# Performance work log

Hardware: AMD Instinct MI355X
Metric: run time of the kernel (lower is better)

Reference implementation:

```python
import jax, jax.numpy as jnp
import numpy as np

R_MIN, R_MAX, MAX_PHASE = 0.9, 0.999, 6.283
BN_EPS = 1e-5


def _lru(x, nu_log, theta_log, B_re, B_im, C_re, C_im, D):
    # x: [B,T,E]; diagonal LRU with complex state of size H
    lam = jnp.exp(-jnp.exp(nu_log) + 1j * jnp.exp(theta_log))          # [H] complex
    gamma = jnp.sqrt(jnp.maximum(1.0 - jnp.abs(lam) ** 2, 1e-12))      # [H]
    Bc = B_re + 1j * B_im                                               # [H,E]
    Cc = C_re + 1j * C_im                                               # [E,H]
    Bu = jnp.einsum('bte,he->bth', x.astype(jnp.complex64), Bc) * gamma  # [B,T,H]

    def step(h, u):
        h = lam * h + u
        return h, h

    h0 = jnp.zeros((x.shape[0], lam.shape[0]), jnp.complex64)
    _, hs = jax.lax.scan(step, h0, jnp.swapaxes(Bu, 0, 1))              # [T,B,H]
    hs = jnp.swapaxes(hs, 0, 1)                                         # [B,T,H]
    return jnp.einsum('bth,eh->bte', hs, Cc).real + D * x               # [B,T,E]


def _batchnorm(x, scale, bias):
    # normalize over (batch, time), feature axis last
    mu = jnp.mean(x, axis=(0, 1))
    var = jnp.var(x, axis=(0, 1))
    return (x - mu) * jax.lax.rsqrt(var + BN_EPS) * scale + bias


def _glu(x):
    a, b = jnp.split(x, 2, axis=-1)
    return a * jax.nn.sigmoid(b)


def setup_inputs() -> dict:
    key = jax.random.key(0)
    ks = jax.random.split(key, 16)
    B, T, TS, E, H, L, O, NB = 32, 2048, 64, 256, 256, 1024, 10, 6
    u1 = jax.random.uniform(ks[0], (NB, H))
    u2 = jax.random.uniform(ks[1], (NB, H))
    nu_log = jnp.log(-0.5 * jnp.log(u1 * (R_MAX**2 - R_MIN**2) + R_MIN**2))
    theta_log = jnp.log(MAX_PHASE * u2)
    return {
        'x': jax.random.normal(ks[2], (B, T, TS), jnp.float32),
        'W_enc': jax.random.normal(ks[3], (TS, E), jnp.float32) / np.sqrt(TS),
        'b_enc': jnp.zeros((E,), jnp.float32),
        'nu_log': nu_log.astype(jnp.float32),
        'theta_log': theta_log.astype(jnp.float32),
        'B_re': jax.random.normal(ks[4], (NB, H, E), jnp.float32) / np.sqrt(2 * E),
        'B_im': jax.random.normal(ks[5], (NB, H, E), jnp.float32) / np.sqrt(2 * E),
        'C_re': jax.random.normal(ks[6], (NB, E, H), jnp.float32) / np.sqrt(H),
        'C_im': jax.random.normal(ks[7], (NB, E, H), jnp.float32) / np.sqrt(H),
        'D': jax.random.normal(ks[8], (NB, E), jnp.float32),
        'W1': jax.random.normal(ks[9], (NB, E, L), jnp.float32) / np.sqrt(E),
        'b1': jnp.zeros((NB, L), jnp.float32),
        'W2': jax.random.normal(ks[10], (NB, L // 2, E), jnp.float32) / np.sqrt(L // 2),
        'b2': jnp.zeros((NB, E), jnp.float32),
        'bn_scale': jnp.ones((NB, E), jnp.float32),
        'bn_bias': jnp.zeros((NB, E), jnp.float32),
        'W_out': jax.random.normal(ks[11], (E, O), jnp.float32) / np.sqrt(E),
        'b_out': jnp.zeros((O,), jnp.float32),
    }


def reference(x, W_enc, b_enc, nu_log, theta_log, B_re, B_im, C_re, C_im, D,
              W1, b1, W2, b2, bn_scale, bn_bias, W_out, b_out):
    x = x @ W_enc + b_enc                      # [B,T,E]
    y = x                                       # residual anchor (same for every block)
    for i in range(6):
        h = _batchnorm(x, bn_scale[i], bn_bias[i])
        h = _lru(h, nu_log[i], theta_log[i], B_re[i], B_im[i], C_re[i], C_im[i], D[i])
        h = _glu(h @ W1[i] + b1[i])             # dropout is identity (p=0 / eval)
        h = h @ W2[i] + b2[i]
        x = h + y
    pooled = jnp.mean(x, axis=1)                # pool=True head: mean over time
    return pooled @ W_out + b_out               # [B, out_dim]
```

## Files before the change

### kernel.cpp

```cpp
#include <hip/hip_runtime.h>
#include <hip/hip_bf16.h>
#include <math.h>

using bf16 = __hip_bfloat16;
typedef __attribute__((ext_vector_type(8))) short s8v;
typedef __attribute__((ext_vector_type(4))) float f4v;

#define MTOT 65536
#define TLEN 2048
#define NCHUNK 32
#define TCH 64

__device__ __forceinline__ float b2f(bf16 x) { return __bfloat162float(x); }
__device__ __forceinline__ bf16 f2b(float x) { return __float2bfloat16(x); }
__device__ __forceinline__ float bits2f(unsigned short u) {
    unsigned int x = ((unsigned int)u) << 16; float f; __builtin_memcpy(&f, &x, 4); return f;
}
__device__ __forceinline__ unsigned short f2bits(float x) {
    bf16 h = f2b(x); unsigned short u; __builtin_memcpy(&u, &h, 2); return u;
}

__device__ __forceinline__ float ldf(const void* p, size_t i, int f) {
    return f ? ((const float*)p)[i] : b2f(((const bf16*)p)[i]);
}

__device__ __forceinline__ void ld_g2l(const void* g, void* l) {
    __builtin_amdgcn_global_load_lds(
        (const __attribute__((address_space(1))) void*)g,
        (__attribute__((address_space(3))) void*)l,
        16, 0, 0);
}

__global__ void detect_k(const unsigned short* __restrict__ x, int* __restrict__ flag) {
    int tid = threadIdx.x;
    int cnt = 0;
    for (int i = tid; i < 8192; i += 256) {
        int e = (x[i] >> 7) & 0xFF;
        if (e == 0 || e == 0xFF) cnt++;
    }
    __shared__ int red[256];
    red[tid] = cnt;
    __syncthreads();
    for (int s = 128; s > 0; s >>= 1) {
        if (tid < s) red[tid] += red[tid + s];
        __syncthreads();
    }
    if (tid == 0) flag[0] = (red[0] >= 2) ? 1 : 0;
}

__global__ void cvt_k(const void* __restrict__ src, bf16* __restrict__ dst, int n,
                      const int* __restrict__ flag) {
    int f = *flag;
    int i = blockIdx.x * 256 + threadIdx.x;
    if (i < n) dst[i] = f2b(ldf(src, i, f));
}

__global__ void cvt_small(const void* b_enc, const void* Dp, const void* b1, const void* b2,
                          const void* bn_s, const void* bn_b, const void* W_out, const void* b_out,
                          bf16* b_encb, bf16* Db, bf16* b1b, bf16* b2b, bf16* bnsb, bf16* bnbb,
                          bf16* Woutb, bf16* boutb, const int* __restrict__ flag) {
    int f = *flag;
    int blk = blockIdx.x, t = threadIdx.x;
    const void* src; bf16* dst; int base, n;
    if (blk < 1)       { src = b_enc; dst = b_encb; base = blk;      n = 256; }
    else if (blk < 7)  { src = Dp;    dst = Db;     base = blk - 1;  n = 1536; }
    else if (blk < 31) { src = b1;    dst = b1b;    base = blk - 7;  n = 6144; }
    else if (blk < 37) { src = b2;    dst = b2b;    base = blk - 31; n = 1536; }
    else if (blk < 43) { src = bn_s;  dst = bnsb;   base = blk - 37; n = 1536; }
    else if (blk < 49) { src = bn_b;  dst = bnbb;   base = blk - 43; n = 1536; }
    else if (blk < 59) { src = W_out; dst = Woutb;  base = blk - 49; n = 2560; }
    else               { src = b_out; dst = boutb;  base = 0;        n = 10; }
    int i = base * 256 + t;
    if (i < n) dst[i] = f2b(ldf(src, i, f));
}

__global__ void lamgam_k(const void* __restrict__ nu, const void* __restrict__ th,
                         float* __restrict__ lamb, float* __restrict__ gamt,
                         const int* __restrict__ flag) {
    int f = *flag;
    int g = blockIdx.x * 256 + threadIdx.x;
    float nl = ldf(nu, g, f), tl = ldf(th, g, f);
    float mag = expf(-expf(nl));
    float ang = expf(tl);
    lamb[g * 2] = mag * cosf(ang);
    lamb[g * 2 + 1] = mag * sinf(ang);
    gamt[g] = sqrtf(fmaxf(1.f - mag * mag, 1e-12f));
}

template<int KK, int NBN, int EPI>
__global__ __launch_bounds__(256)
void gemm_v7(const bf16* __restrict__ A, const bf16* __restrict__ W,
             bf16* __restrict__ outB, bf16* __restrict__ outB2, int ldo,
             const bf16* __restrict__ bias,
             const bf16* __restrict__ Dv, const bf16* __restrict__ aux,
             const float* __restrict__ fstats, float* __restrict__ spart)
{
    constexpr int LG = (NBN == 8) ? 3 : 2;
    const int id = blockIdx.x;
    const int xcd = id & 7, q = id >> 3;
    const int bn = q & (NBN - 1);
    const int bm = (q >> LG) * 8 + xcd;

    const int tid = threadIdx.x;
    const int lane = tid & 63, wv = tid >> 6;
    const int wm = wv >> 1, wn = wv & 1;
    const int quad = lane >> 4, cl = lane & 15;

    __shared__ __align__(16) short As[3][128 * 32];
    __shared__ __align__(16) short Ws[3][64 * 32];
    __shared__ float sred[256];

    const char* Ab = (const char*)A + (size_t)bm * 128 * ((size_t)KK * 2);
    const char* Wb = (const char*)W + (size_t)bn * 64 * ((size_t)KK * 2);
    constexpr int ldb = KK * 2;

    auto stage = [&](int t, int bi) {
        const int kb = t * 64;
#pragma unroll
        for (int it = 0; it < 2; ++it) {
            int G = it * 256 + tid;
            int r = G >> 2;
            int gl = (G & 3) ^ ((r >> 1) & 3);
            ld_g2l(Ab + (size_t)r * ldb + kb + gl * 16,
                   (char*)As[bi] + (it * 4 + wv) * 1024);
        }
        {
            int r = tid >> 2;
            int gl = (tid & 3) ^ ((r >> 1) & 3);
            ld_g2l(Wb + (size_t)r * ldb + kb + gl * 16,
                   (char*)Ws[bi] + wv * 1024);
        }
    };

    f4v acc[4][2];
#pragma unroll
    for (int i = 0; i < 4; i++)
#pragma unroll
        for (int j = 0; j < 2; j++) acc[i][j] = (f4v){0.f, 0.f, 0.f, 0.f};

    constexpr int NT = KK >> 5;
    stage(0, 0);
    if (NT > 1) stage(1, 1);
#pragma unroll
    for (int t = 0; t < NT; ++t) {
        if (t + 2 < NT) {
            stage(t + 2, (t + 2) % 3);
            asm volatile("s_waitcnt vmcnt(6)" ::: "memory");
        } else if (t + 1 < NT) {
            asm volatile("s_waitcnt vmcnt(3)" ::: "memory");
        } else {
            asm volatile("s_waitcnt vmcnt(0)" ::: "memory");
        }
        asm volatile("s_barrier" ::: "memory");
        const char* Ac = (const char*)As[t % 3];
        const char* Wc = (const char*)Ws[t % 3];
        s8v af[4], bw[2];
#pragma unroll
        for (int i = 0; i < 4; i++) {
            int r = wm * 64 + i * 16 + cl;
            af[i] = *(const s8v*)(Ac + r * 64 + ((quad ^ ((r >> 1) & 3)) * 16));
        }
#pragma unroll
        for (int j = 0; j < 2; j++) {
            int r = wn * 32 + j * 16 + cl;
            bw[j] = *(const s8v*)(Wc + r * 64 + ((quad ^ ((r >> 1) & 3)) * 16));
        }
#pragma unroll
        for (int i = 0; i < 4; i++)
#pragma unroll
            for (int j = 0; j < 2; j++)
                acc[i][j] = __builtin_amdgcn_mfma_f32_16x16x32_bf16(af[i], bw[j], acc[i][j], 0, 0, 0);
        asm volatile("s_barrier" ::: "memory");
    }

    const size_t ld = (size_t)ldo;
    constexpr bool STATS = (EPI == 1 || EPI == 5);
#pragma unroll
    for (int j = 0; j < 2; j++) {
        float ss = 0.f, ss2 = 0.f;
        const int n = bn * 64 + wn * 32 + j * 16 + cl;
#pragma unroll
        for (int i = 0; i < 4; i++) {
#pragma unroll
            for (int r4 = 0; r4 < 4; r4++) {
                int m = bm * 128 + wm * 64 + i * 16 + quad * 4 + r4;
                size_t idx = (size_t)m * ld + n;
                float v = acc[i][j][r4];
                if (EPI == 1) {
                    v += b2f(bias[n]);
                    outB[idx] = f2b(v);
                    outB2[idx] = f2b(v);
                } else if (EPI == 2) {
                    v += b2f(Dv[n]) * (fstats[n] * b2f(aux[idx]) + fstats[256 + n]);
                    outB[idx] = f2b(v);
                } else if (EPI == 5) {
                    v += b2f(bias[n]) + b2f(aux[idx]);
                    outB[idx] = f2b(v);
                } else if (EPI == 6) {
                    v += fstats[n];
                    outB[idx] = f2b(v);
                }
                if (STATS) { ss += v; ss2 += v * v; }
            }
        }
        if (STATS) {
            ss += __shfl_xor(ss, 16);  ss += __shfl_xor(ss, 32);
            ss2 += __shfl_xor(ss2, 16); ss2 += __shfl_xor(ss2, 32);
            if (lane < 16) {
                int nl = wn * 32 + j * 16 + lane;
                sred[wm * 64 + nl] = ss;
                sred[128 + wm * 64 + nl] = ss2;
            }
        }
    }
    if constexpr (STATS) {
        __syncthreads();
        if (tid < 64) {
            float sv = sred[tid] + sred[64 + tid];
            float sv2 = sred[128 + tid] + sred[192 + tid];
            spart[(size_t)bm * 256 + bn * 64 + tid] = sv;
            spart[131072 + (size_t)bm * 256 + bn * 64 + tid] = sv2;
        }
    }
}

__global__ __launch_bounds__(256)
void glu_v7(const bf16* __restrict__ A, const bf16* __restrict__ W,
            bf16* __restrict__ outB, const bf16* __restrict__ bias)
{
    constexpr int KK = 256;
    const int id = blockIdx.x;
    const int xcd = id & 7, q = id >> 3;
    const int nb = q & 7;
    const int bm = (q >> 3) * 8 + xcd;

    const int tid = threadIdx.x;
    const int lane = tid & 63, wv = tid >> 6;
    const int wm = wv >> 1, wn = wv & 1;
    const int quad = lane >> 4, cl = lane & 15;

    __shared__ __align__(16) short As[3][128 * 32];
    __shared__ __align__(16) short Vs[3][64 * 32];
    __shared__ __align__(16) short Gs[3][64 * 32];

    const char* Ab = (const char*)A + (size_t)bm * 128 * ((size_t)KK * 2);
    const char* Vb = (const char*)W + (size_t)(nb * 64) * ((size_t)KK * 2);
    const char* Gb = (const char*)W + (size_t)(512 + nb * 64) * ((size_t)KK * 2);
    constexpr int ldb = KK * 2;

    auto stage = [&](int t, int bi) {
        const int kb = t * 64;
#pragma unroll
        for (int it = 0; it < 2; ++it) {
            int G = it * 256 + tid;
            int r = G >> 2;
            int gl = (G & 3) ^ ((r >> 1) & 3);
            ld_g2l(Ab + (size_t)r * ldb + kb + gl * 16,
                   (char*)As[bi] + (it * 4 + wv) * 1024);
        }
        {
            int r = tid >> 2;
            int gl = (tid & 3) ^ ((r >> 1) & 3);
            ld_g2l(Vb + (size_t)r * ldb + kb + gl * 16, (char*)Vs[bi] + wv * 1024);
            ld_g2l(Gb + (size_t)r * ldb + kb + gl * 16, (char*)Gs[bi] + wv * 1024);
        }
    };

    f4v accv[4][2], accg[4][2];
#pragma unroll
    for (int i = 0; i < 4; i++)
#pragma unroll
        for (int j = 0; j < 2; j++) {
            accv[i][j] = (f4v){0.f, 0.f, 0.f, 0.f};
            accg[i][j] = (f4v){0.f, 0.f, 0.f, 0.f};
        }

    constexpr int NT = KK >> 5;
    stage(0, 0);
    stage(1, 1);
#pragma unroll
    for (int t = 0; t < NT; ++t) {
        if (t + 2 < NT) {
            stage(t + 2, (t + 2) % 3);
            asm volatile("s_waitcnt vmcnt(8)" ::: "memory");
        } else if (t + 1 < NT) {
            asm volatile("s_waitcnt vmcnt(4)" ::: "memory");
        } else {
            asm volatile("s_waitcnt vmcnt(0)" ::: "memory");
        }
        asm volatile("s_barrier" ::: "memory");
        const char* Ac = (const char*)As[t % 3];
        const char* Vc = (const char*)Vs[t % 3];
        const char* Gc = (const char*)Gs[t % 3];
        s8v af[4], bv[2], bg[2];
#pragma unroll
        for (int i = 0; i < 4; i++) {
            int r = wm * 64 + i * 16 + cl;
            af[i] = *(const s8v*)(Ac + r * 64 + ((quad ^ ((r >> 1) & 3)) * 16));
        }
#pragma unroll
        for (int j = 0; j < 2; j++) {
            int r = wn * 32 + j * 16 + cl;
            int off = r * 64 + ((quad ^ ((r >> 1) & 3)) * 16);
            bv[j] = *(const s8v*)(Vc + off);
            bg[j] = *(const s8v*)(Gc + off);
        }
#pragma unroll
        for (int i = 0; i < 4; i++)
#pragma unroll
            for (int j = 0; j < 2; j++) {
                accv[i][j] = __builtin_amdgcn_mfma_f32_16x16x32_bf16(af[i], bv[j], accv[i][j], 0, 0, 0);
                accg[i][j] = __builtin_amdgcn_mfma_f32_16x16x32_bf16(af[i], bg[j], accg[i][j], 0, 0, 0);
            }
        asm volatile("s_barrier" ::: "memory");
    }

#pragma unroll
    for (int i = 0; i < 4; i++) {
#pragma unroll
        for (int j = 0; j < 2; j++) {
#pragma unroll
            for (int r4 = 0; r4 < 4; r4++) {
                int m = bm * 128 + wm * 64 + i * 16 + quad * 4 + r4;
                int n = nb * 64 + wn * 32 + j * 16 + cl;
                float v = accv[i][j][r4] + b2f(bias[n]);
                float g = accg[i][j][r4] + b2f(bias[512 + n]);
                outB[(size_t)m * 512 + n] = f2b(v * (1.f / (1.f + __expf(-g))));
            }
        }
    }
}

__global__ void bn_finish2(const float* __restrict__ part, float* __restrict__ stats,
                           const bf16* __restrict__ sc, const bf16* __restrict__ bi) {
    int e = blockIdx.x;
    int t = threadIdx.x;
    float s = part[(size_t)t * 256 + e] + part[(size_t)(t + 256) * 256 + e];
    float s2 = part[131072 + (size_t)t * 256 + e] + part[131072 + (size_t)(t + 256) * 256 + e];
    __shared__ float rs[256], rs2[256];
    rs[t] = s; rs2[t] = s2;
    __syncthreads();
    for (int k = 128; k > 0; k >>= 1) {
        if (t < k) { rs[t] += rs[t + k]; rs2[t] += rs2[t + k]; }
        __syncthreads();
    }
    if (t == 0) {
        float mu = rs[0] * (1.f / 65536.f);
        float var = rs2[0] * (1.f / 65536.f) - mu * mu;
        float a = rsqrtf(var + 1e-5f) * b2f(sc[e]);
        stats[e] = a;
        stats[256 + e] = b2f(bi[e]) - mu * a;
    }
}

__global__ void pack_wb(const void* __restrict__ B_re, const void* __restrict__ B_im,
                        size_t off, const float* __restrict__ gam,
                        const float* __restrict__ stats,
                        bf16* __restrict__ out, float* __restrict__ bias_out,
                        const int* __restrict__ flag) {
    int f = *flag;
    int n = blockIdx.x;
    int e = threadIdx.x;
    int h = n >> 1;
    const void* src = (n & 1) ? B_im : B_re;
    float v = ldf(src, off + (size_t)h * 256 + e, f);
    out[(size_t)n * 256 + e] = f2b(v * gam[h] * stats[e]);
    __shared__ float rs[256];
    rs[e] = v * stats[256 + e];
    __syncthreads();
    for (int k = 128; k > 0; k >>= 1) {
        if (e < k) rs[e] += rs[e + k];
        __syncthreads();
    }
    if (e == 0) bias_out[n] = rs[0] * gam[h];
}

__global__ void pack_all(const void* __restrict__ C_re, const void* __restrict__ C_im,
                         const void* __restrict__ W1, const void* __restrict__ W2,
                         bf16* __restrict__ wc6, bf16* __restrict__ w1t6, bf16* __restrict__ w2t6,
                         const int* __restrict__ flag) {
    int f = *flag;
    int L = blockIdx.x >> 11;
    int blk = blockIdx.x & 2047;
    size_t offC = (size_t)L * 65536, offW1 = (size_t)L * 262144, offW2 = (size_t)L * 131072;
    if (blk < 512) {
        int g = blk * 256 + threadIdx.x;
        int e = g >> 9, k = g & 511, h = k >> 1;
        float v = ldf((k & 1) ? C_im : C_re, offC + (size_t)e * 256 + h, f);
        wc6[(size_t)L * 131072 + g] = f2b((k & 1) ? -v : v);
    } else if (blk < 1536) {
        int g = (blk - 512) * 256 + threadIdx.x;
        int n = g >> 8, k = g & 255;
        w1t6[(size_t)L * 262144 + g] = f2b(ldf(W1, offW1 + (size_t)k * 1024 + n, f));
    } else {
        int g = (blk - 1536) * 256 + threadIdx.x;
        int n = g >> 9, k = g & 511;
        w2t6[(size_t)L * 131072 + g] = f2b(ldf(W2, offW2 + (size_t)k * 256 + n, f));
    }
}

__global__ void lru_carry(const bf16* __restrict__ bu, const float* __restrict__ lam,
                          float* __restrict__ carry) {
    int gg = blockIdx.x * 256 + threadIdx.x;
    int hp = gg & 127, c = (gg >> 7) & 31, b = gg >> 12;
    f4v lm = *(const f4v*)&lam[hp * 4];
    float sr0 = 0.f, si0 = 0.f, sr1 = 0.f, si1 = 0.f;
    const char* p = (const char*)(bu + ((size_t)(b * TLEN + c * TCH)) * 512) + hp * 8;
    for (int t = 0; t < TCH; t++) {
        unsigned long long u = *(const unsigned long long*)p;
        float ur0 = bits2f((unsigned short)u), ui0 = bits2f((unsigned short)(u >> 16));
        float ur1 = bits2f((unsigned short)(u >> 32)), ui1 = bits2f((unsigned short)(u >> 48));
        float nr0 = lm[0] * sr0 - lm[1] * si0 + ur0;
        si0 = lm[0] * si0 + lm[1] * sr0 + ui0; sr0 = nr0;
        float nr1 = lm[2] * sr1 - lm[3] * si1 + ur1;
        si1 = lm[2] * si1 + lm[3] * sr1 + ui1; sr1 = nr1;
        p += 1024;
    }
    *(f4v*)&carry[(size_t)gg * 4] = (f4v){sr0, si0, sr1, si1};
}

__global__ void lru_prefix(const float* __restrict__ carry, float* __restrict__ pre,
                           const float* __restrict__ lam) {
    int g = blockIdx.x * 256 + threadIdx.x;
    int h = g & 255, b = g >> 8;
    float pr = lam[h * 2], pi = lam[h * 2 + 1];
    for (int k = 0; k < 6; k++) { float nr = pr * pr - pi * pi; pi = 2.f * pr * pi; pr = nr; }
    float er = 0.f, ei = 0.f;
    for (int c = 0; c < NCHUNK; c++) {
        size_t idx = ((size_t)(b * NCHUNK + c) * 256 + h) * 2;
        pre[idx] = er; pre[idx + 1] = ei;
        float cr = carry[idx], ci = carry[idx + 1];
        float nr = pr * er - pi * ei + cr;
        ei = pr * ei + pi * er + ci;
        er = nr;
    }
}

__global__ void lru_final(bf16* __restrict__ bu, const float* __restrict__ pre,
                          const float* __restrict__ lam) {
    int gg = blockIdx.x * 256 + threadIdx.x;
    int hp = gg & 127, c = (gg >> 7) & 31, b = gg >> 12;
    f4v lm = *(const f4v*)&lam[hp * 4];
    f4v st = *(const f4v*)&pre[(size_t)gg * 4];
    float sr0 = st[0], si0 = st[1], sr1 = st[2], si1 = st[3];
    char* p = (char*)(bu + ((size_t)(b * TLEN + c * TCH)) * 512) + hp * 8;
    for (int t = 0; t < TCH; t++) {
        unsigned long long u = *(const unsigned long long*)p;
        float ur0 = bits2f((unsigned short)u), ui0 = bits2f((unsigned short)(u >> 16));
        float ur1 = bits2f((unsigned short)(u >> 32)), ui1 = bits2f((unsigned short)(u >> 48));
        float nr0 = lm[0] * sr0 - lm[1] * si0 + ur0;
        si0 = lm[0] * si0 + lm[1] * sr0 + ui0; sr0 = nr0;
        float nr1 = lm[2] * sr1 - lm[3] * si1 + ur1;
        si1 = lm[2] * si1 + lm[3] * sr1 + ui1; sr1 = nr1;
        unsigned long long w = (unsigned long long)f2bits(sr0)
                             | ((unsigned long long)f2bits(si0) << 16)
                             | ((unsigned long long)f2bits(sr1) << 32)
                             | ((unsigned long long)f2bits(si1) << 48);
        *(unsigned long long*)p = w;
        p += 1024;
    }
}

__global__ void head_k(const float* __restrict__ part, const bf16* __restrict__ W_out,
                       const bf16* __restrict__ b_out, void* __restrict__ out,
                       const int* __restrict__ flag) {
    int b = blockIdx.x;
    int tid = threadIdx.x;
    __shared__ float sp[256];
    __shared__ float red[160];
    float s = 0.f;
    for (int c = 0; c < 16; c++) s += part[((size_t)(b * 16 + c)) * 256 + tid];
    sp[tid] = s * (1.f / 2048.f);
    __syncthreads();
    if (tid < 160) {
        int o = tid >> 4, sg = tid & 15;
        float a = 0.f;
        for (int e = sg; e < 256; e += 16) a += sp[e] * b2f(W_out[e * 10 + o]);
        red[tid] = a;
    }
    __syncthreads();
    if (tid < 10) {
        float acc = b2f(b_out[tid]);
        for (int sg = 0; sg < 16; sg++) acc += red[tid * 16 + sg];
        if (*flag) ((float*)out)[b * 10 + tid] = acc;
        else       ((bf16*)out)[b * 10 + tid] = f2b(acc);
    }
}

__global__ void pack_wt_enc(const void* __restrict__ W_enc, bf16* __restrict__ out,
                            const int* __restrict__ flag) {
    int f = *flag;
    int g = blockIdx.x * 256 + threadIdx.x;
    int n = g >> 6, k = g & 63;
    out[g] = f2b(ldf(W_enc, (size_t)k * 256 + n, f));
}

extern "C" void kernel_launch(void* const* d_in, const int* in_sizes, int n_in,
                              void* d_out, int out_size, void* d_ws, size_t ws_size,
                              hipStream_t stream) {
    (void)in_sizes; (void)n_in; (void)out_size; (void)ws_size;
    const void* x      = d_in[0];
    const void* W_enc  = d_in[1];
    const void* b_enc  = d_in[2];
    const void* nu_log = d_in[3];
    const void* th_log = d_in[4];
    const void* B_re   = d_in[5];
    const void* B_im   = d_in[6];
    const void* C_re   = d_in[7];
    const void* C_im   = d_in[8];
    const void* Dp     = d_in[9];
    const void* W1     = d_in[10];
    const void* b1     = d_in[11];
    const void* W2     = d_in[12];
    const void* b2     = d_in[13];
    const void* bn_s   = d_in[14];
    const void* bn_b   = d_in[15];
    const void* W_out  = d_in[16];
    const void* b_out  = d_in[17];

    char* w = (char*)d_ws;
    bf16* xc  = (bf16*)w; w += (size_t)MTOT * 256 * 2;
    bf16* y   = (bf16*)w; w += (size_t)MTOT * 256 * 2;
    bf16* hbn = (bf16*)w; w += (size_t)MTOT * 256 * 2;
    bf16* bu  = (bf16*)w; w += (size_t)MTOT * 512 * 2;
    float* stats  = (float*)w; w += 4096;
    float* bnpart = (float*)w; w += 1048576;
    float* carry  = (float*)w; w += 2097152;
    float* pre    = (float*)w; w += 2097152;
    float* lamb   = (float*)w; w += 12288;
    float* gamt   = (float*)w; w += 6144;
    float* bubias = (float*)w; w += 2048;
    int*   flag   = (int*)w;  w += 256;
    bf16* wt_enc = (bf16*)w; w += 32768;
    bf16* wb   = (bf16*)w; w += 262144;
    bf16* wc6  = (bf16*)w; w += 6 * 262144;
    bf16* w1t6 = (bf16*)w; w += 6 * 524288;
    bf16* w2t6 = (bf16*)w; w += 6 * 262144;
    bf16* b_encb = (bf16*)w; w += 512;
    bf16* Db     = (bf16*)w; w += 3072;
    bf16* b1b    = (bf16*)w; w += 12288;
    bf16* b2b    = (bf16*)w; w += 3072;
    bf16* bnsb   = (bf16*)w; w += 3072;
    bf16* bnbb   = (bf16*)w; w += 3072;
    bf16* Woutb  = (bf16*)w; w += 5120;
    bf16* boutb  = (bf16*)w; w += 32;
    bf16* xb = bu;

    dim3 blk(256);
    detect_k<<<1, blk, 0, stream>>>((const unsigned short*)x, flag);
    cvt_k<<<16384, blk, 0, stream>>>(x, xb, 4194304, flag);
    cvt_small<<<60, blk, 0, stream>>>(b_enc, Dp, b1, b2, bn_s, bn_b, W_out, b_out,
                                      b_encb, Db, b1b, b2b, bnsb, bnbb, Woutb, boutb, flag);
    lamgam_k<<<6, blk, 0, stream>>>(nu_log, th_log, lamb, gamt, flag);
    pack_wt_enc<<<64, blk, 0, stream>>>(W_enc, wt_enc, flag);
    pack_all<<<12288, blk, 0, stream>>>(C_re, C_im, W1, W2, wc6, w1t6, w2t6, flag);

    gemm_v7<64, 4, 1><<<2048, blk, 0, stream>>>(xb, wt_enc, xc, y, 256,
                                                b_encb, nullptr, nullptr, nullptr, bnpart);
    for (int i = 0; i < 6; ++i) {
        bn_finish2<<<256, blk, 0, stream>>>(bnpart, stats, bnsb + i * 256, bnbb + i * 256);
        pack_wb<<<512, blk, 0, stream>>>(B_re, B_im, (size_t)i * 65536, gamt + i * 256,
                                         stats, wb, bubias, flag);
        gemm_v7<256, 8, 6><<<4096, blk, 0, stream>>>(xc, wb, bu, nullptr, 512,
                                                     nullptr, nullptr, nullptr, bubias, nullptr);
        lru_carry<<<512, blk, 0, stream>>>(bu, lamb + i * 512, carry);
        lru_prefix<<<32, blk, 0, stream>>>(carry, pre, lamb + i * 512);
        lru_final<<<512, blk, 0, stream>>>(bu, pre, lamb + i * 512);
        gemm_v7<512, 4, 2><<<2048, blk, 0, stream>>>(bu, wc6 + (size_t)i * 131072, hbn, nullptr, 256,
                                                     nullptr, Db + i * 256, xc, stats, nullptr);
        glu_v7<<<4096, blk, 0, stream>>>(hbn, w1t6 + (size_t)i * 262144, bu, b1b + i * 1024);
        gemm_v7<512, 4, 5><<<2048, blk, 0, stream>>>(bu, w2t6 + (size_t)i * 131072, xc, nullptr, 256,
                                                     b2b + i * 256, nullptr, y, nullptr, bnpart);
    }
    head_k<<<32, blk, 0, stream>>>(bnpart, Woutb, boutb, d_out, flag);
}
```

Before: 1.393 ms.

## Process two M-tiles per GEMM block with continuous cross-tile prefetch pipeline

Each GEMM and GLU block now handles two consecutive 128-row M tiles. The three-stage LDS pipeline runs across both tiles, so the second tile's loads are prefetched while the first tile finishes and its epilogue is written. Grids are halved to match. The input conversion kernel also handles four elements per thread. The aim is to amortize pipeline fill/drain and launch overhead, at the cost of fewer blocks and a mid-loop epilogue that may lengthen the critical path.

```diff
diff --git a/kernel.cpp b/kernel.cpp
--- a/kernel.cpp
+++ b/kernel.cpp
@@ -48,11 +48,16 @@
     if (tid == 0) flag[0] = (red[0] >= 2) ? 1 : 0;
 }
 
-__global__ void cvt_k(const void* __restrict__ src, bf16* __restrict__ dst, int n,
-                      const int* __restrict__ flag) {
+__global__ void cvt_k4(const void* __restrict__ src, bf16* __restrict__ dst, int n,
+                       const int* __restrict__ flag) {
     int f = *flag;
-    int i = blockIdx.x * 256 + threadIdx.x;
-    if (i < n) dst[i] = f2b(ldf(src, i, f));
+    int i = (blockIdx.x * 256 + threadIdx.x) * 4;
+    if (i + 3 < n) {
+#pragma unroll
+        for (int k = 0; k < 4; k++) dst[i + k] = f2b(ldf(src, i + k, f));
+    } else {
+        for (int k = 0; k < 4 && i + k < n; k++) dst[i + k] = f2b(ldf(src, i + k, f));
+    }
 }
 
 __global__ void cvt_small(const void* b_enc, const void* Dp, const void* b1, const void* b2,
@@ -89,17 +94,21 @@
 
 template<int KK, int NBN, int EPI>
 __global__ __launch_bounds__(256)
-void gemm_v7(const bf16* __restrict__ A, const bf16* __restrict__ W,
+void gemm_v8(const bf16* __restrict__ A, const bf16* __restrict__ W,
              bf16* __restrict__ outB, bf16* __restrict__ outB2, int ldo,
              const bf16* __restrict__ bias,
              const bf16* __restrict__ Dv, const bf16* __restrict__ aux,
              const float* __restrict__ fstats, float* __restrict__ spart)
 {
     constexpr int LG = (NBN == 8) ? 3 : 2;
+    constexpr int NT = KK >> 5;
+    constexpr int LOG2NT = (KK == 64) ? 1 : (KK == 256) ? 3 : 4;
+    constexpr int GT = 2 * NT;
+
     const int id = blockIdx.x;
     const int xcd = id & 7, q = id >> 3;
     const int bn = q & (NBN - 1);
-    const int bm = (q >> LG) * 8 + xcd;
+    const int mgrp = (q >> LG) * 8 + xcd;
 
     const int tid = threadIdx.x;
     const int lane = tid & 63, wv = tid >> 6;
@@ -110,17 +119,20 @@
     __shared__ __align__(16) short Ws[3][64 * 32];
     __shared__ float sred[256];
 
-    const char* Ab = (const char*)A + (size_t)bm * 128 * ((size_t)KK * 2);
+    const char* Abase = (const char*)A;
     const char* Wb = (const char*)W + (size_t)bn * 64 * ((size_t)KK * 2);
     constexpr int ldb = KK * 2;
 
-    auto stage = [&](int t, int bi) {
-        const int kb = t * 64;
+    auto stage = [&](int G) {
+        const int tile = G >> LOG2NT;
+        const int kb = (G & (NT - 1)) * 64;
+        const int bi = G % 3;
+        const char* Ab = Abase + (size_t)(mgrp * 2 + tile) * 128 * ((size_t)KK * 2);
 #pragma unroll
         for (int it = 0; it < 2; ++it) {
-            int G = it * 256 + tid;
-            int r = G >> 2;
-            int gl = (G & 3) ^ ((r >> 1) & 3);
+            int Gt = it * 256 + tid;
+            int r = Gt >> 2;
+            int gl = (Gt & 3) ^ ((r >> 1) & 3);
             ld_g2l(Ab + (size_t)r * ldb + kb + gl * 16,
                    (char*)As[bi] + (it * 4 + wv) * 1024);
         }
@@ -138,22 +150,24 @@
 #pragma unroll
         for (int j = 0; j < 2; j++) acc[i][j] = (f4v){0.f, 0.f, 0.f, 0.f};
 
-    constexpr int NT = KK >> 5;
-    stage(0, 0);
-    if (NT > 1) stage(1, 1);
-#pragma unroll
-    for (int t = 0; t < NT; ++t) {
-        if (t + 2 < NT) {
-            stage(t + 2, (t + 2) % 3);
+    const size_t ld = (size_t)ldo;
+    constexpr bool STATS = (EPI == 1 || EPI == 5);
+
+    stage(0);
+    stage(1);
+#pragma unroll
+    for (int G = 0; G < GT; ++G) {
+        if (G + 2 < GT) {
+            stage(G + 2);
             asm volatile("s_waitcnt vmcnt(6)" ::: "memory");
-        } else if (t + 1 < NT) {
+        } else if (G + 1 < GT) {
             asm volatile("s_waitcnt vmcnt(3)" ::: "memory");
         } else {
             asm volatile("s_waitcnt vmcnt(0)" ::: "memory");
         }
         asm volatile("s_barrier" ::: "memory");
-        const char* Ac = (const char*)As[t % 3];
-        const char* Wc = (const char*)Ws[t % 3];
+        const char* Ac = (const char*)As[G % 3];
+        const char* Wc = (const char*)Ws[G % 3];
         s8v af[4], bw[2];
 #pragma unroll
         for (int i = 0; i < 4; i++) {
@@ -171,68 +185,76 @@
             for (int j = 0; j < 2; j++)
                 acc[i][j] = __builtin_amdgcn_mfma_f32_16x16x32_bf16(af[i], bw[j], acc[i][j], 0, 0, 0);
         asm volatile("s_barrier" ::: "memory");
-    }
-
-    const size_t ld = (size_t)ldo;
-    constexpr bool STATS = (EPI == 1 || EPI == 5);
-#pragma unroll
-    for (int j = 0; j < 2; j++) {
-        float ss = 0.f, ss2 = 0.f;
-        const int n = bn * 64 + wn * 32 + j * 16 + cl;
-#pragma unroll
-        for (int i = 0; i < 4; i++) {
-#pragma unroll
-            for (int r4 = 0; r4 < 4; r4++) {
-                int m = bm * 128 + wm * 64 + i * 16 + quad * 4 + r4;
-                size_t idx = (size_t)m * ld + n;
-                float v = acc[i][j][r4];
-                if (EPI == 1) {
-                    v += b2f(bias[n]);
-                    outB[idx] = f2b(v);
-                    outB2[idx] = f2b(v);
-                } else if (EPI == 2) {
-                    v += b2f(Dv[n]) * (fstats[n] * b2f(aux[idx]) + fstats[256 + n]);
-                    outB[idx] = f2b(v);
-                } else if (EPI == 5) {
-                    v += b2f(bias[n]) + b2f(aux[idx]);
-                    outB[idx] = f2b(v);
-                } else if (EPI == 6) {
-                    v += fstats[n];
-                    outB[idx] = f2b(v);
+
+        if ((G & (NT - 1)) == NT - 1) {
+            const int bm = mgrp * 2 + (G >> LOG2NT);
+#pragma unroll
+            for (int j = 0; j < 2; j++) {
+                float ss = 0.f, ss2 = 0.f;
+                const int n = bn * 64 + wn * 32 + j * 16 + cl;
+#pragma unroll
+                for (int i = 0; i < 4; i++) {
+#pragma unroll
+                    for (int r4 = 0; r4 < 4; r4++) {
+                        int m = bm * 128 + wm * 64 + i * 16 + quad * 4 + r4;
+                        size_t idx = (size_t)m * ld + n;
+                        float v = acc[i][j][r4];
+                        if (EPI == 1) {
+                            v += b2f(bias[n]);
+                            outB[idx] = f2b(v);
+                            outB2[idx] = f2b(v);
+                        } else if (EPI == 2) {
+                            v += b2f(Dv[n]) * (fstats[n] * b2f(aux[idx]) + fstats[256 + n]);
+                            outB[idx] = f2b(v);
+                        } else if (EPI == 5) {
+                            v += b2f(bias[n]) + b2f(aux[idx]);
+                            outB[idx] = f2b(v);
+                        } else if (EPI == 6) {
+                            v += fstats[n];
+                            outB[idx] = f2b(v);
+                        }
+                        if (STATS) { ss += v; ss2 += v * v; }
+                    }
                 }
-                if (STATS) { ss += v; ss2 += v * v; }
+                if (STATS) {
+                    ss += __shfl_xor(ss, 16);  ss += __shfl_xor(ss, 32);
+                    ss2 += __shfl_xor(ss2, 16); ss2 += __shfl_xor(ss2, 32);
+                    if (lane < 16) {
+                        int nl = wn * 32 + j * 16 + lane;
+                        sred[wm * 64 + nl] = ss;
+                        sred[128 + wm * 64 + nl] = ss2;
+                    }
+                }
             }
-        }
-        if (STATS) {
-            ss += __shfl_xor(ss, 16);  ss += __shfl_xor(ss, 32);
-            ss2 += __shfl_xor(ss2, 16); ss2 += __shfl_xor(ss2, 32);
-            if (lane < 16) {
-                int nl = wn * 32 + j * 16 + lane;
-                sred[wm * 64 + nl] = ss;
-                sred[128 + wm * 64 + nl] = ss2;
+            if constexpr (STATS) {
+                __syncthreads();
+                if (tid < 64) {
+                    float sv = sred[tid] + sred[64 + tid];
+                    float sv2 = sred[128 + tid] + sred[192 + tid];
+                    spart[(size_t)bm * 256 + bn * 64 + tid] = sv;
+                    spart[131072 + (size_t)bm * 256 + bn * 64 + tid] = sv2;
+                }
             }
-        }
-    }
-    if constexpr (STATS) {
-        __syncthreads();
-        if (tid < 64) {
-            float sv = sred[tid] + sred[64 + tid];
-            float sv2 = sred[128 + tid] + sred[192 + tid];
-            spart[(size_t)bm * 256 + bn * 64 + tid] = sv;
-            spart[131072 + (size_t)bm * 256 + bn * 64 + tid] = sv2;
+            if (G + 1 < GT) {
+#pragma unroll
+                for (int i = 0; i < 4; i++)
+#pragma unroll
+                    for (int j = 0; j < 2; j++) acc[i][j] = (f4v){0.f, 0.f, 0.f, 0.f};
+            }
         }
     }
 }
 
 __global__ __launch_bounds__(256)
-void glu_v7(const bf16* __restrict__ A, const bf16* __restrict__ W,
+void glu_v8(const bf16* __restrict__ A, const bf16* __restrict__ W,
             bf16* __restrict__ outB, const bf16* __restrict__ bias)
 {
     constexpr int KK = 256;
+    constexpr int NT = 8, GT = 16;
     const int id = blockIdx.x;
     const int xcd = id & 7, q = id >> 3;
     const int nb = q & 7;
-    const int bm = (q >> 3) * 8 + xcd;
+    const int mgrp = (q >> 3) * 8 + xcd;
 
     const int tid = threadIdx.x;
     const int lane = tid & 63, wv = tid >> 6;
@@ -243,18 +265,21 @@
     __shared__ __align__(16) short Vs[3][64 * 32];
     __shared__ __align__(16) short Gs[3][64 * 32];
 
-    const char* Ab = (const char*)A + (size_t)bm * 128 * ((size_t)KK * 2);
+    const char* Abase = (const char*)A;
     const char* Vb = (const char*)W + (size_t)(nb * 64) * ((size_t)KK * 2);
     const char* Gb = (const char*)W + (size_t)(512 + nb * 64) * ((size_t)KK * 2);
     constexpr int ldb = KK * 2;
 
-    auto stage = [&](int t, int bi) {
-        const int kb = t * 64;
+    auto stage = [&](int G) {
+        const int tile = G >> 3;
+        const int kb = (G & 7) * 64;
+        const int bi = G % 3;
+        const char* Ab = Abase + (size_t)(mgrp * 2 + tile) * 128 * ((size_t)KK * 2);
 #pragma unroll
         for (int it = 0; it < 2; ++it) {
-            int G = it * 256 + tid;
-            int r = G >> 2;
-            int gl = (G & 3) ^ ((r >> 1) & 3);
+            int Gt = it * 256 + tid;
+            int r = Gt >> 2;
+            int gl = (Gt & 3) ^ ((r >> 1) & 3);
             ld_g2l(Ab + (size_t)r * ldb + kb + gl * 16,
                    (char*)As[bi] + (it * 4 + wv) * 1024);
         }
@@ -275,23 +300,22 @@
             accg[i][j] = (f4v){0.f, 0.f, 0.f, 0.f};
         }
 
-    constexpr int NT = KK >> 5;
-    stage(0, 0);
-    stage(1, 1);
-#pragma unroll
-    for (int t = 0; t < NT; ++t) {
-        if (t + 2 < NT) {
-            stage(t + 2, (t + 2) % 3);
+    stage(0);
+    stage(1);
+#pragma unroll
+    for (int G = 0; G < GT; ++G) {
+        if (G + 2 < GT) {
+            stage(G + 2);
             asm volatile("s_waitcnt vmcnt(8)" ::: "memory");
-        } else if (t + 1 < NT) {
+        } else if (G + 1 < GT) {
             asm volatile("s_waitcnt vmcnt(4)" ::: "memory");
         } else {
             asm volatile("s_waitcnt vmcnt(0)" ::: "memory");
         }
         asm volatile("s_barrier" ::: "memory");
-        const char* Ac = (const char*)As[t % 3];
-        const char* Vc = (const char*)Vs[t % 3];
-        const char* Gc = (const char*)Gs[t % 3];
+        const char* Ac = (const char*)As[G % 3];
+        const char* Vc = (const char*)Vs[G % 3];
+        const char* Gc = (const char*)Gs[G % 3];
         s8v af[4], bv[2], bg[2];
 #pragma unroll
         for (int i = 0; i < 4; i++) {
@@ -313,19 +337,31 @@
                 accg[i][j] = __builtin_amdgcn_mfma_f32_16x16x32_bf16(af[i], bg[j], accg[i][j], 0, 0, 0);
             }
         asm volatile("s_barrier" ::: "memory");
-    }
-
-#pragma unroll
-    for (int i = 0; i < 4; i++) {
-#pragma unroll
-        for (int j = 0; j < 2; j++) {
-#pragma unroll
-            for (int r4 = 0; r4 < 4; r4++) {
-                int m = bm * 128 + wm * 64 + i * 16 + quad * 4 + r4;
-                int n = nb * 64 + wn * 32 + j * 16 + cl;
-                float v = accv[i][j][r4] + b2f(bias[n]);
-                float g = accg[i][j][r4] + b2f(bias[512 + n]);
-                outB[(size_t)m * 512 + n] = f2b(v * (1.f / (1.f + __expf(-g))));
+
+        if ((G & 7) == 7) {
+            const int bm = mgrp * 2 + (G >> 3);
+#pragma unroll
+            for (int i = 0; i < 4; i++) {
+#pragma unroll
+                for (int j = 0; j < 2; j++) {
+#pragma unroll
+                    for (int r4 = 0; r4 < 4; r4++) {
+                        int m = bm * 128 + wm * 64 + i * 16 + quad * 4 + r4;
+                        int n = nb * 64 + wn * 32 + j * 16 + cl;
+                        float v = accv[i][j][r4] + b2f(bias[n]);
+                        float g = accg[i][j][r4] + b2f(bias[512 + n]);
+                        outB[(size_t)m * 512 + n] = f2b(v * (1.f / (1.f + __expf(-g))));
+                    }
+                }
+            }
+            if (G + 1 < GT) {
+#pragma unroll
+                for (int i = 0; i < 4; i++)
+#pragma unroll
+                    for (int j = 0; j < 2; j++) {
+                        accv[i][j] = (f4v){0.f, 0.f, 0.f, 0.f};
+                        accg[i][j] = (f4v){0.f, 0.f, 0.f, 0.f};
+                    }
             }
         }
     }
@@ -548,28 +584,28 @@
 
     dim3 blk(256);
     detect_k<<<1, blk, 0, stream>>>((const unsigned short*)x, flag);
-    cvt_k<<<16384, blk, 0, stream>>>(x, xb, 4194304, flag);
+    cvt_k4<<<4096, blk, 0, stream>>>(x, xb, 4194304, flag);
     cvt_small<<<60, blk, 0, stream>>>(b_enc, Dp, b1, b2, bn_s, bn_b, W_out, b_out,
                                       b_encb, Db, b1b, b2b, bnsb, bnbb, Woutb, boutb, flag);
     lamgam_k<<<6, blk, 0, stream>>>(nu_log, th_log, lamb, gamt, flag);
     pack_wt_enc<<<64, blk, 0, stream>>>(W_enc, wt_enc, flag);
     pack_all<<<12288, blk, 0, stream>>>(C_re, C_im, W1, W2, wc6, w1t6, w2t6, flag);
 
-    gemm_v7<64, 4, 1><<<2048, blk, 0, stream>>>(xb, wt_enc, xc, y, 256,
+    gemm_v8<64, 4, 1><<<1024, blk, 0, stream>>>(xb, wt_enc, xc, y, 256,
                                                 b_encb, nullptr, nullptr, nullptr, bnpart);
     for (int i = 0; i < 6; ++i) {
         bn_finish2<<<256, blk, 0, stream>>>(bnpart, stats, bnsb + i * 256, bnbb + i * 256);
         pack_wb<<<512, blk, 0, stream>>>(B_re, B_im, (size_t)i * 65536, gamt + i * 256,
                                          stats, wb, bubias, flag);
-        gemm_v7<256, 8, 6><<<4096, blk, 0, stream>>>(xc, wb, bu, nullptr, 512,
+        gemm_v8<256, 8, 6><<<2048, blk, 0, stream>>>(xc, wb, bu, nullptr, 512,
                                                      nullptr, nullptr, nullptr, bubias, nullptr);
         lru_carry<<<512, blk, 0, stream>>>(bu, lamb + i * 512, carry);
         lru_prefix<<<32, blk, 0, stream>>>(carry, pre, lamb + i * 512);
         lru_final<<<512, blk, 0, stream>>>(bu, pre, lamb + i * 512);
-        gemm_v7<512, 4, 2><<<2048, blk, 0, stream>>>(bu, wc6 + (size_t)i * 131072, hbn, nullptr, 256,
+        gemm_v8<512, 4, 2><<<1024, blk, 0, stream>>>(bu, wc6 + (size_t)i * 131072, hbn, nullptr, 256,
                                                      nullptr, Db + i * 256, xc, stats, nullptr);
-        glu_v7<<<4096, blk, 0, stream>>>(hbn, w1t6 + (size_t)i * 262144, bu, b1b + i * 1024);
-        gemm_v7<512, 4, 5><<<2048, blk, 0, stream>>>(bu, w2t6 + (size_t)i * 131072, xc, nullptr, 256,
+        glu_v8<<<2048, blk, 0, stream>>>(hbn, w1t6 + (size_t)i * 262144, bu, b1b + i * 1024);
+        gemm_v8<512, 4, 5><<<1024, blk, 0, stream>>>(bu, w2t6 + (size_t)i * 131072, xc, nullptr, 256,
                                                      b2b + i * 256, nullptr, y, nullptr, bnpart);
     }
     head_k<<<32, blk, 0, stream>>>(bnpart, Woutb, boutb, d_out, flag);
```

After: 1.507 ms. 1.08x slower.

## Fuse LRU chunk carry computation into the Bu GEMM epilogue

Applied to the files above, without the earlier changes.

Removes the separate lru_carry kernel. The Bu projection GEMM epilogue now computes each 64-step chunk's end state as a weighted sum of its outputs, using powers of lambda built in registers, then reduces with wave shuffles and writes the carry directly. This saves a full re-read of the Bu tensor and one launch per block. The cost is extra epilogue arithmetic and register pressure, and the carry is now a power-weighted sum rather than a sequential recurrence, which may round differently.

```diff
diff --git a/kernel.cpp b/kernel.cpp
--- a/kernel.cpp
+++ b/kernel.cpp
@@ -93,7 +93,8 @@
              bf16* __restrict__ outB, bf16* __restrict__ outB2, int ldo,
              const bf16* __restrict__ bias,
              const bf16* __restrict__ Dv, const bf16* __restrict__ aux,
-             const float* __restrict__ fstats, float* __restrict__ spart)
+             const float* __restrict__ fstats, float* __restrict__ spart,
+             const float* __restrict__ lamp, float* __restrict__ carry)
 {
     constexpr int LG = (NBN == 8) ? 3 : 2;
     const int id = blockIdx.x;
@@ -179,6 +180,33 @@
     for (int j = 0; j < 2; j++) {
         float ss = 0.f, ss2 = 0.f;
         const int n = bn * 64 + wn * 32 + j * 16 + cl;
+        float Er[4], Ei[4], Cr[4], Cim[4];
+        if constexpr (EPI == 6) {
+            int h = n >> 1;
+            float lr = lamp[h * 2], li = lamp[h * 2 + 1];
+            float a2r = lr * lr - li * li, a2i = 2.f * lr * li;
+            float a3r = a2r * lr - a2i * li, a3i = a2r * li + a2i * lr;
+            float l4r = a2r * a2r - a2i * a2i, l4i = 2.f * a2r * a2i;
+            float l8r = l4r * l4r - l4i * l4i, l8i = 2.f * l4r * l4i;
+            float l12r = l8r * l4r - l8i * l4i, l12i = l8r * l4i + l8i * l4r;
+            float Br = (quad == 0) ? l12r : (quad == 1) ? l8r : (quad == 2) ? l4r : 1.f;
+            float Bi = (quad == 0) ? l12i : (quad == 1) ? l8i : (quad == 2) ? l4i : 0.f;
+            float Ar[4] = { a3r, a2r, lr, 1.f };
+            float Ai[4] = { a3i, a2i, li, 0.f };
+#pragma unroll
+            for (int r4 = 0; r4 < 4; r4++) {
+                Er[r4] = Ar[r4] * Br - Ai[r4] * Bi;
+                Ei[r4] = Ar[r4] * Bi + Ai[r4] * Br;
+            }
+            float l16r = l12r * l4r - l12i * l4i, l16i = l12r * l4i + l12i * l4r;
+            float l32r = l16r * l16r - l16i * l16i, l32i = 2.f * l16r * l16i;
+            float l48r = l32r * l16r - l32i * l16i, l48i = l32r * l16i + l32i * l16r;
+            Cr[0] = l48r; Cim[0] = l48i;
+            Cr[1] = l32r; Cim[1] = l32i;
+            Cr[2] = l16r; Cim[2] = l16i;
+            Cr[3] = 1.f;  Cim[3] = 0.f;
+        }
+        float Sr = 0.f, Si = 0.f;
 #pragma unroll
         for (int i = 0; i < 4; i++) {
 #pragma unroll
@@ -198,9 +226,26 @@
                     outB[idx] = f2b(v);
                 } else if (EPI == 6) {
                     v += fstats[n];
-                    outB[idx] = f2b(v);
+                    bf16 ob = f2b(v);
+                    outB[idx] = ob;
+                    float vr = b2f(ob);
+                    float wr = Er[r4] * Cr[i] - Ei[r4] * Cim[i];
+                    float wi = Er[r4] * Cim[i] + Ei[r4] * Cr[i];
+                    Sr += vr * wr;
+                    Si += vr * wi;
                 }
                 if (STATS) { ss += v; ss2 += v * v; }
+            }
+        }
+        if constexpr (EPI == 6) {
+            Sr += __shfl_xor(Sr, 16); Sr += __shfl_xor(Sr, 32);
+            Si += __shfl_xor(Si, 16); Si += __shfl_xor(Si, 32);
+            float pSr = __shfl_xor(Sr, 1), pSi = __shfl_xor(Si, 1);
+            if (quad == 0 && (cl & 1) == 0) {
+                size_t gc = (size_t)(bm * 2 + wm);
+                size_t ci = (gc * 256 + (size_t)(n >> 1)) * 2;
+                carry[ci]     = Sr - pSi;
+                carry[ci + 1] = Si + pSr;
             }
         }
         if (STATS) {
@@ -397,26 +442,6 @@
         int n = g >> 9, k = g & 511;
         w2t6[(size_t)L * 131072 + g] = f2b(ldf(W2, offW2 + (size_t)k * 256 + n, f));
     }
-}
-
-__global__ void lru_carry(const bf16* __restrict__ bu, const float* __restrict__ lam,
-                          float* __restrict__ carry) {
-    int gg = blockIdx.x * 256 + threadIdx.x;
-    int hp = gg & 127, c = (gg >> 7) & 31, b = gg >> 12;
-    f4v lm = *(const f4v*)&lam[hp * 4];
-    float sr0 = 0.f, si0 = 0.f, sr1 = 0.f, si1 = 0.f;
-    const char* p = (const char*)(bu + ((size_t)(b * TLEN + c * TCH)) * 512) + hp * 8;
-    for (int t = 0; t < TCH; t++) {
-        unsigned long long u = *(const unsigned long long*)p;
-        float ur0 = bits2f((unsigned short)u), ui0 = bits2f((unsigned short)(u >> 16));
-        float ur1 = bits2f((unsigned short)(u >> 32)), ui1 = bits2f((unsigned short)(u >> 48));
-        float nr0 = lm[0] * sr0 - lm[1] * si0 + ur0;
-        si0 = lm[0] * si0 + lm[1] * sr0 + ui0; sr0 = nr0;
-        float nr1 = lm[2] * sr1 - lm[3] * si1 + ur1;
-        si1 = lm[2] * si1 + lm[3] * sr1 + ui1; sr1 = nr1;
-        p += 1024;
-    }
-    *(f4v*)&carry[(size_t)gg * 4] = (f4v){sr0, si0, sr1, si1};
 }
 
 __global__ void lru_prefix(const float* __restrict__ carry, float* __restrict__ pre,
@@ -556,21 +581,24 @@
     pack_all<<<12288, blk, 0, stream>>>(C_re, C_im, W1, W2, wc6, w1t6, w2t6, flag);
 
     gemm_v7<64, 4, 1><<<2048, blk, 0, stream>>>(xb, wt_enc, xc, y, 256,
-                                                b_encb, nullptr, nullptr, nullptr, bnpart);
+                                                b_encb, nullptr, nullptr, nullptr, bnpart,
+                                                nullptr, nullptr);
     for (int i = 0; i < 6; ++i) {
         bn_finish2<<<256, blk, 0, stream>>>(bnpart, stats, bnsb + i * 256, bnbb + i * 256);
         pack_wb<<<512, blk, 0, stream>>>(B_re, B_im, (size_t)i * 65536, gamt + i * 256,
                                          stats, wb, bubias, flag);
         gemm_v7<256, 8, 6><<<4096, blk, 0, stream>>>(xc, wb, bu, nullptr, 512,
-                                                     nullptr, nullptr, nullptr, bubias, nullptr);
-        lru_carry<<<512, blk, 0, stream>>>(bu, lamb + i * 512, carry);
+                                                     nullptr, nullptr, nullptr, bubias, nullptr,
+                                                     lamb + i * 512, carry);
         lru_prefix<<<32, blk, 0, stream>>>(carry, pre, lamb + i * 512);
         lru_final<<<512, blk, 0, stream>>>(bu, pre, lamb + i * 512);
         gemm_v7<512, 4, 2><<<2048, blk, 0, stream>>>(bu, wc6 + (size_t)i * 131072, hbn, nullptr, 256,
-                                                     nullptr, Db + i * 256, xc, stats, nullptr);
+                                                     nullptr, Db + i * 256, xc, stats, nullptr,
+                                                     nullptr, nullptr);
         glu_v7<<<4096, blk, 0, stream>>>(hbn, w1t6 + (size_t)i * 262144, bu, b1b + i * 1024);
         gemm_v7<512, 4, 5><<<2048, blk, 0, stream>>>(bu, w2t6 + (size_t)i * 131072, xc, nullptr, 256,
-                                                     b2b + i * 256, nullptr, y, nullptr, bnpart);
+                                                     b2b + i * 256, nullptr, y, nullptr, bnpart,
+                                                     nullptr, nullptr);
     }
     head_k<<<32, blk, 0, stream>>>(bnpart, Woutb, boutb, d_out, flag);
 }
```

After: 1.390 ms. Within noise of the previous version (-0.2%).
